# Optimization experiments

Hardware: AMD Instinct MI355X
Metric: run time of the kernel (lower is better)

Reference implementation:

```python
import jax, jax.numpy as jnp
import numpy as np

DIM = 256
NEG_SLOPE = 0.01  # torch F.leaky_relu default


def setup_inputs() -> dict:
    key = jax.random.key(0)
    ks = jax.random.split(key, 10)
    B, O, I, D = 16, 64, 512, DIM
    q = jax.random.normal(ks[0], (B, O, D), dtype=jnp.float32)
    k = jax.random.normal(ks[1], (B, I, D), dtype=jnp.float32)
    v = jax.random.normal(ks[2], (B, I, D), dtype=jnp.float32)
    mask = jax.random.randint(ks[3], (B, I), 0, 2).astype(bool)  # 1/True = pad
    s = 1.0 / np.sqrt(2 * D)
    # score MLP: Linear(2D -> D), tanh, Linear(D -> 1)
    W1 = jax.random.normal(ks[4], (D, 2 * D), dtype=jnp.float32) * s
    b1 = jnp.zeros((D,), dtype=jnp.float32)
    W2 = jax.random.normal(ks[5], (1, D), dtype=jnp.float32) * (1.0 / np.sqrt(D))
    b2 = jnp.zeros((1,), dtype=jnp.float32)
    # output projection fw: Linear(D -> D)
    Wf = jax.random.normal(ks[6], (D, D), dtype=jnp.float32) * (1.0 / np.sqrt(D))
    bf = jnp.zeros((D,), dtype=jnp.float32)
    return {"q": q, "k": k, "v": v, "mask": mask,
            "W1": W1, "b1": b1, "W2": W2, "b2": b2, "Wf": Wf, "bf": bf}


def reference(q, k, v, mask, W1, b1, W2, b2, Wf, bf):
    # Linear over concat([q, k]) decomposes exactly: W1 @ [q;k] = W1q@q + W1k@k
    D = q.shape[-1]
    W1q, W1k = W1[:, :D], W1[:, D:]
    qp = jnp.einsum('bod,hd->boh', q, W1q)          # (B, O, D)
    kp = jnp.einsum('bid,hd->bih', k, W1k)          # (B, I, D)
    h = jnp.tanh(qp[:, :, None, :] + kp[:, None, :, :] + b1)  # (B, O, I, D)
    score = jnp.einsum('boih,h->boi', h, W2[0]) + b2[0]       # (B, O, I)
    score = jnp.where(mask[:, None, :], -jnp.inf, score)
    attn = jax.nn.softmax(score, axis=-1)           # (B, O, I)
    out = jnp.einsum('boi,bid->bod', attn, v)       # (B, O, D)
    out = out @ Wf.T + bf                           # dropout in eval mode = identity
    out = jnp.where(out >= 0, out, NEG_SLOPE * out) # leaky_relu
    return out, attn
```

## Files before the change

### kernel.cpp

```cpp
#include <hip/hip_runtime.h>
#include <math.h>

#define DIM 256
#define BATCH 16
#define NO 64
#define NI 512
#define NEG_SLOPE 0.01f
#define CSCALE 2.885390081777927f
#define OT 2

__global__ __launch_bounds__(256, 4) void proj_kernel(
    const float* __restrict__ q, const float* __restrict__ k,
    const float* __restrict__ W1, const float* __restrict__ b1,
    const float* __restrict__ Wf,
    float* __restrict__ Eq, float* __restrict__ Ek4, float* __restrict__ WfT)
{
  __shared__ float smem[8704];

  const int t  = threadIdx.x;
  const int bx = blockIdx.x;

  if (bx >= 576) {
    const int tt = bx - 576;
    const int tr = tt >> 2, tc = tt & 3;
#pragma unroll
    for (int p = 0; p < 4; ++p) {
      int idx = p * 256 + t;
      int row = idx >> 4, j = idx & 15;
      float4 vv = *(const float4*)(Wf + (size_t)(tr * 64 + row) * 256 + tc * 64 + j * 4);
      *(float4*)&smem[row * 68 + j * 4] = vv;
    }
    __syncthreads();
#pragma unroll
    for (int p = 0; p < 4; ++p) {
      int idx = p * 256 + t;
      int row = idx >> 4, j = idx & 15;
      float4 ov;
      ov.x = smem[(j * 4 + 0) * 68 + row];
      ov.y = smem[(j * 4 + 1) * 68 + row];
      ov.z = smem[(j * 4 + 2) * 68 + row];
      ov.w = smem[(j * 4 + 3) * 68 + row];
      *(float4*)(WfT + (size_t)(tc * 64 + row) * 256 + tr * 64 + j * 4) = ov;
    }
    return;
  }

  float* At = smem;
  float* Wt = smem + 4352;

  const int tx = t & 15;
  const int ty = t >> 4;
  const int mt = bx >> 2;
  const int nt = bx & 3;
  const int r0 = mt * 64;
  const int h0 = nt * 64;
  const bool isq = (r0 < BATCH * NO);
  const float* src = isq ? (q + (size_t)r0 * DIM)
                         : (k + (size_t)(r0 - BATCH * NO) * DIM);
  const int coff = isq ? 0 : DIM;

  float acc[4][4] = {};

  for (int c0 = 0; c0 < DIM; c0 += 64) {
    __syncthreads();
#pragma unroll
    for (int p = 0; p < 4; ++p) {
      int idx = p * 256 + t;
      int row = idx >> 4, j = idx & 15;
      float4 av = *(const float4*)(src + (size_t)row * DIM + c0 + j * 4);
      At[(4 * j + 0) * 68 + row] = av.x;
      At[(4 * j + 1) * 68 + row] = av.y;
      At[(4 * j + 2) * 68 + row] = av.z;
      At[(4 * j + 3) * 68 + row] = av.w;
      float4 wv = *(const float4*)(W1 + (size_t)(h0 + row) * (2 * DIM) + coff + c0 + j * 4);
      Wt[(4 * j + 0) * 68 + row] = wv.x;
      Wt[(4 * j + 1) * 68 + row] = wv.y;
      Wt[(4 * j + 2) * 68 + row] = wv.z;
      Wt[(4 * j + 3) * 68 + row] = wv.w;
    }
    __syncthreads();
#pragma unroll
    for (int dk = 0; dk < 64; ++dk) {
      float4 a4 = *(const float4*)&At[dk * 68 + ty * 4];
      float4 w4 = *(const float4*)&Wt[dk * 68 + tx * 4];
      const float ar[4] = {a4.x, a4.y, a4.z, a4.w};
      const float wr[4] = {w4.x, w4.y, w4.z, w4.w};
#pragma unroll
      for (int rr = 0; rr < 4; ++rr)
#pragma unroll
        for (int cc = 0; cc < 4; ++cc)
          acc[rr][cc] = fmaf(ar[rr], wr[cc], acc[rr][cc]);
    }
  }

  if (isq) {
    float4 bv = *(const float4*)(b1 + h0 + tx * 4);
    const float br[4] = {bv.x, bv.y, bv.z, bv.w};
#pragma unroll
    for (int rr = 0; rr < 4; ++rr) {
      int r = r0 + ty * 4 + rr;
      float4 ov;
      ov.x = __builtin_amdgcn_exp2f((acc[rr][0] + br[0]) * CSCALE);
      ov.y = __builtin_amdgcn_exp2f((acc[rr][1] + br[1]) * CSCALE);
      ov.z = __builtin_amdgcn_exp2f((acc[rr][2] + br[2]) * CSCALE);
      ov.w = __builtin_amdgcn_exp2f((acc[rr][3] + br[3]) * CSCALE);
      *(float4*)(Eq + (size_t)r * DIM + h0 + tx * 4) = ov;
    }
  } else {
    int ig0 = r0 - BATCH * NO;
    int b   = ig0 >> 9;
    int i0  = (ig0 & 511) + ty * 4;
    int hq0 = (h0 >> 2) + tx;
#pragma unroll
    for (int rr = 0; rr < 4; ++rr) {
      float4 ov;
      ov.x = __builtin_amdgcn_exp2f(acc[rr][0] * CSCALE);
      ov.y = __builtin_amdgcn_exp2f(acc[rr][1] * CSCALE);
      ov.z = __builtin_amdgcn_exp2f(acc[rr][2] * CSCALE);
      ov.w = __builtin_amdgcn_exp2f(acc[rr][3] * CSCALE);
      *(float4*)(Ek4 + ((size_t)(b * 64 + hq0) * NI + i0 + rr) * 4) = ov;
    }
  }
}

__device__ __forceinline__ void f4arr(float4 v, float* a) {
  a[0] = v.x; a[1] = v.y; a[2] = v.z; a[3] = v.w;
}

__global__ __launch_bounds__(512, 4) void attn_kernel(
    const float* __restrict__ Eq, const float* __restrict__ Ek4,
    const float* __restrict__ v, const int* __restrict__ mask,
    const float* __restrict__ W2, const float* __restrict__ b2,
    const float* __restrict__ WfT, const float* __restrict__ bf,
    float* __restrict__ out, float* __restrict__ attn_out)
{
  __shared__ float sc[OT][NI];
  __shared__ float pvp[8][OT][DIM];
  __shared__ float o0[OT][DIM];
  __shared__ float red4[8][OT];
  __shared__ float redw[8];

  const int t    = threadIdx.x;
  const int lane = t & 63;
  const int wid  = t >> 6;

  const int blk  = blockIdx.x;
  const int tile = (blk & 7) * 64 + (blk >> 3);
  const int b    = tile >> 5;
  const int bo0  = b * 64 + (tile & 31) * OT;

  float partial = (t < DIM) ? W2[t] : 0.f;
#pragma unroll
  for (int off = 32; off >= 1; off >>= 1) partial += __shfl_xor(partial, off, 64);
  if (lane == 0) redw[wid] = partial;
  __syncthreads();
  float sumw2 = 0.f;
#pragma unroll
  for (int w = 0; w < 8; ++w) sumw2 += redw[w];
  const float base = sumw2 + b2[0];

  const int i = t;
  const float4* kb4 = (const float4*)Ek4 + (size_t)b * 64 * NI;
  const float* qrow0 = Eq + (size_t)(bo0 + 0) * DIM;
  const float* qrow1 = Eq + (size_t)(bo0 + 1) * DIM;

  float acc0 = 0.f, acc1 = 0.f;
#pragma unroll 8
  for (int hq = 0; hq < 64; ++hq) {
    float4 kq = kb4[(size_t)hq * NI + i];
    float wr[4], q0r[4], q1r[4], kv[4];
    f4arr(*(const float4*)(W2 + hq * 4), wr);
    f4arr(*(const float4*)(qrow0 + hq * 4), q0r);
    f4arr(*(const float4*)(qrow1 + hq * 4), q1r);
    f4arr(kq, kv);
#pragma unroll
    for (int pr = 0; pr < 2; ++pr) {
      const int ea = pr * 2, eb = pr * 2 + 1;
      float A0 = fmaf(q0r[ea], kv[ea], 1.f);
      float B0 = fmaf(q0r[eb], kv[eb], 1.f);
      float N0 = fmaf(wr[eb], A0, wr[ea] * B0);
      acc0 = fmaf(N0, __builtin_amdgcn_rcpf(A0 * B0), acc0);
      float A1 = fmaf(q1r[ea], kv[ea], 1.f);
      float B1 = fmaf(q1r[eb], kv[eb], 1.f);
      float N1 = fmaf(wr[eb], A1, wr[ea] * B1);
      acc1 = fmaf(N1, __builtin_amdgcn_rcpf(A1 * B1), acc1);
    }
  }

  const int mv = mask[(size_t)b * NI + i];
  float s0 = base - 2.f * acc0;
  float s1 = base - 2.f * acc1;
  if (mv) { s0 = -INFINITY; s1 = -INFINITY; }

  float p0 = __builtin_amdgcn_exp2f(s0 * 1.4426950408889634f);
  float p1 = __builtin_amdgcn_exp2f(s1 * 1.4426950408889634f);
  float ps0 = p0, ps1 = p1;
#pragma unroll
  for (int off = 32; off >= 1; off >>= 1) {
    ps0 += __shfl_xor(ps0, off, 64);
    ps1 += __shfl_xor(ps1, off, 64);
  }
  __syncthreads();
  if (lane == 0) { red4[wid][0] = ps0; red4[wid][1] = ps1; }
  __syncthreads();
  float ss0 = 0.f, ss1 = 0.f;
#pragma unroll
  for (int w = 0; w < 8; ++w) { ss0 += red4[w][0]; ss1 += red4[w][1]; }
  const float a0 = p0 * __builtin_amdgcn_rcpf(ss0);
  const float a1 = p1 * __builtin_amdgcn_rcpf(ss1);
  sc[0][i] = a0;
  sc[1][i] = a1;
  attn_out[(size_t)(bo0 + 0) * NI + i] = a0;
  attn_out[(size_t)(bo0 + 1) * NI + i] = a1;
  __syncthreads();

  {
    const int d4 = lane;
    float4 av0 = {0.f, 0.f, 0.f, 0.f};
    float4 av1 = {0.f, 0.f, 0.f, 0.f};
    const float4* vb4 = (const float4*)(v + (size_t)b * NI * DIM);
#pragma unroll 2
    for (int ib = wid * 64; ib < wid * 64 + 64; ib += 4) {
      float sa0[4], sa1[4];
      f4arr(*(const float4*)&sc[0][ib], sa0);
      f4arr(*(const float4*)&sc[1][ib], sa1);
#pragma unroll
      for (int j = 0; j < 4; ++j) {
        float4 vv = vb4[(size_t)(ib + j) * 64 + d4];
        av0.x = fmaf(sa0[j], vv.x, av0.x);
        av0.y = fmaf(sa0[j], vv.y, av0.y);
        av0.z = fmaf(sa0[j], vv.z, av0.z);
        av0.w = fmaf(sa0[j], vv.w, av0.w);
        av1.x = fmaf(sa1[j], vv.x, av1.x);
        av1.y = fmaf(sa1[j], vv.y, av1.y);
        av1.z = fmaf(sa1[j], vv.z, av1.z);
        av1.w = fmaf(sa1[j], vv.w, av1.w);
      }
    }
    *(float4*)&pvp[wid][0][d4 * 4] = av0;
    *(float4*)&pvp[wid][1][d4 * 4] = av1;
  }
  __syncthreads();
  {
    int oo = t >> 8, d = t & 255;
    float sacc = 0.f;
#pragma unroll
    for (int w = 0; w < 8; ++w) sacc += pvp[w][oo][d];
    o0[oo][d] = sacc;
  }
  __syncthreads();

  if (t < DIM) {
    const int d = t;
    float f0 = 0.f, f1 = 0.f;
#pragma unroll 8
    for (int e4 = 0; e4 < 64; ++e4) {
      float oa[4], ob[4];
      f4arr(*(const float4*)&o0[0][e4 * 4], oa);
      f4arr(*(const float4*)&o0[1][e4 * 4], ob);
#pragma unroll
      for (int c = 0; c < 4; ++c) {
        float wv = WfT[(size_t)(e4 * 4 + c) * DIM + d];
        f0 = fmaf(oa[c], wv, f0);
        f1 = fmaf(ob[c], wv, f1);
      }
    }
    float bfv = bf[d];
    f0 += bfv; f1 += bfv;
    f0 = (f0 >= 0.f) ? f0 : NEG_SLOPE * f0;
    f1 = (f1 >= 0.f) ? f1 : NEG_SLOPE * f1;
    out[(size_t)(bo0 + 0) * DIM + d] = f0;
    out[(size_t)(bo0 + 1) * DIM + d] = f1;
  }
}

extern "C" void kernel_launch(void* const* d_in, const int* in_sizes, int n_in,
                              void* d_out, int out_size, void* d_ws, size_t ws_size,
                              hipStream_t stream) {
  const float* q    = (const float*)d_in[0];
  const float* k    = (const float*)d_in[1];
  const float* v    = (const float*)d_in[2];
  const int*   mask = (const int*)d_in[3];
  const float* W1   = (const float*)d_in[4];
  const float* b1   = (const float*)d_in[5];
  const float* W2   = (const float*)d_in[6];
  const float* b2   = (const float*)d_in[7];
  const float* Wf   = (const float*)d_in[8];
  const float* bf   = (const float*)d_in[9];

  float* out      = (float*)d_out;
  float* attn_out = out + (size_t)BATCH * NO * DIM;

  float* Eq  = (float*)d_ws;
  float* Ek4 = Eq + (size_t)BATCH * NO * DIM;
  float* WfT = Ek4 + (size_t)BATCH * DIM * NI;

  proj_kernel<<<592, 256, 0, stream>>>(q, k, W1, b1, Wf, Eq, Ek4, WfT);
  attn_kernel<<<(BATCH * NO) / OT, 512, 0, stream>>>(Eq, Ek4, v, mask, W2, b2,
                                                     WfT, bf, out, attn_out);
}
```

Measured before the change: 142.4 us.

## Process four query rows per attention block with 1024 threads

Each attention block now handles four output rows instead of two, using 1024 threads split into two halves that each compute scores for two rows. The V-weighted sum and the output projection then reuse every V and WfT load across four rows, halving the global traffic for those operands. In exchange the grid shrinks to 256 blocks with one block per CU allowed, and the score phase still reads Ek4 separately in each half, so occupancy and latency hiding may drop.

After: 153.9 us. 8.1% more time.

```diff
diff --git a/kernel.cpp b/kernel.cpp
--- a/kernel.cpp
+++ b/kernel.cpp
@@ -7,7 +7,6 @@
 #define NI 512
 #define NEG_SLOPE 0.01f
 #define CSCALE 2.885390081777927f
-#define OT 2
 
 __global__ __launch_bounds__(256, 4) void proj_kernel(
     const float* __restrict__ q, const float* __restrict__ k,
@@ -127,27 +126,29 @@
   a[0] = v.x; a[1] = v.y; a[2] = v.z; a[3] = v.w;
 }
 
-__global__ __launch_bounds__(512, 4) void attn_kernel(
+__global__ __launch_bounds__(1024, 1) void attn_kernel(
     const float* __restrict__ Eq, const float* __restrict__ Ek4,
     const float* __restrict__ v, const int* __restrict__ mask,
     const float* __restrict__ W2, const float* __restrict__ b2,
     const float* __restrict__ WfT, const float* __restrict__ bf,
     float* __restrict__ out, float* __restrict__ attn_out)
 {
-  __shared__ float sc[OT][NI];
-  __shared__ float pvp[8][OT][DIM];
-  __shared__ float o0[OT][DIM];
-  __shared__ float red4[8][OT];
-  __shared__ float redw[8];
+  __shared__ float sc[4][NI];
+  __shared__ float pvp[16][4][DIM];
+  __shared__ float o0[4][DIM];
+  __shared__ float red4[16][2];
+  __shared__ float redw[16];
 
   const int t    = threadIdx.x;
   const int lane = t & 63;
   const int wid  = t >> 6;
+  const int half = t >> 9;
+  const int i    = t & 511;
 
   const int blk  = blockIdx.x;
-  const int tile = (blk & 7) * 64 + (blk >> 3);
-  const int b    = tile >> 5;
-  const int bo0  = b * 64 + (tile & 31) * OT;
+  const int tile = (blk & 7) * 32 + (blk >> 3);
+  const int b    = tile >> 4;
+  const int bo0  = b * 64 + (tile & 15) * 4;
 
   float partial = (t < DIM) ? W2[t] : 0.f;
 #pragma unroll
@@ -156,13 +157,12 @@
   __syncthreads();
   float sumw2 = 0.f;
 #pragma unroll
-  for (int w = 0; w < 8; ++w) sumw2 += redw[w];
+  for (int w = 0; w < 16; ++w) sumw2 += redw[w];
   const float base = sumw2 + b2[0];
 
-  const int i = t;
   const float4* kb4 = (const float4*)Ek4 + (size_t)b * 64 * NI;
-  const float* qrow0 = Eq + (size_t)(bo0 + 0) * DIM;
-  const float* qrow1 = Eq + (size_t)(bo0 + 1) * DIM;
+  const float* qrow0 = Eq + (size_t)(bo0 + half * 2 + 0) * DIM;
+  const float* qrow1 = Eq + (size_t)(bo0 + half * 2 + 1) * DIM;
 
   float acc0 = 0.f, acc1 = 0.f;
 #pragma unroll 8
@@ -205,72 +205,83 @@
   __syncthreads();
   float ss0 = 0.f, ss1 = 0.f;
 #pragma unroll
-  for (int w = 0; w < 8; ++w) { ss0 += red4[w][0]; ss1 += red4[w][1]; }
+  for (int w = 0; w < 8; ++w) {
+    ss0 += red4[half * 8 + w][0];
+    ss1 += red4[half * 8 + w][1];
+  }
   const float a0 = p0 * __builtin_amdgcn_rcpf(ss0);
   const float a1 = p1 * __builtin_amdgcn_rcpf(ss1);
-  sc[0][i] = a0;
-  sc[1][i] = a1;
-  attn_out[(size_t)(bo0 + 0) * NI + i] = a0;
-  attn_out[(size_t)(bo0 + 1) * NI + i] = a1;
+  sc[half * 2 + 0][i] = a0;
+  sc[half * 2 + 1][i] = a1;
+  attn_out[(size_t)(bo0 + half * 2 + 0) * NI + i] = a0;
+  attn_out[(size_t)(bo0 + half * 2 + 1) * NI + i] = a1;
   __syncthreads();
 
   {
     const int d4 = lane;
-    float4 av0 = {0.f, 0.f, 0.f, 0.f};
-    float4 av1 = {0.f, 0.f, 0.f, 0.f};
+    float4 av[4];
+#pragma unroll
+    for (int oo = 0; oo < 4; ++oo) av[oo] = make_float4(0.f, 0.f, 0.f, 0.f);
     const float4* vb4 = (const float4*)(v + (size_t)b * NI * DIM);
 #pragma unroll 2
-    for (int ib = wid * 64; ib < wid * 64 + 64; ib += 4) {
-      float sa0[4], sa1[4];
-      f4arr(*(const float4*)&sc[0][ib], sa0);
-      f4arr(*(const float4*)&sc[1][ib], sa1);
+    for (int ib = wid * 32; ib < wid * 32 + 32; ib += 4) {
+      float sa[4][4];
+#pragma unroll
+      for (int oo = 0; oo < 4; ++oo) f4arr(*(const float4*)&sc[oo][ib], sa[oo]);
 #pragma unroll
       for (int j = 0; j < 4; ++j) {
         float4 vv = vb4[(size_t)(ib + j) * 64 + d4];
-        av0.x = fmaf(sa0[j], vv.x, av0.x);
-        av0.y = fmaf(sa0[j], vv.y, av0.y);
-        av0.z = fmaf(sa0[j], vv.z, av0.z);
-        av0.w = fmaf(sa0[j], vv.w, av0.w);
-        av1.x = fmaf(sa1[j], vv.x, av1.x);
-        av1.y = fmaf(sa1[j], vv.y, av1.y);
-        av1.z = fmaf(sa1[j], vv.z, av1.z);
-        av1.w = fmaf(sa1[j], vv.w, av1.w);
+#pragma unroll
+        for (int oo = 0; oo < 4; ++oo) {
+          av[oo].x = fmaf(sa[oo][j], vv.x, av[oo].x);
+          av[oo].y = fmaf(sa[oo][j], vv.y, av[oo].y);
+          av[oo].z = fmaf(sa[oo][j], vv.z, av[oo].z);
+          av[oo].w = fmaf(sa[oo][j], vv.w, av[oo].w);
+        }
       }
     }
-    *(float4*)&pvp[wid][0][d4 * 4] = av0;
-    *(float4*)&pvp[wid][1][d4 * 4] = av1;
+#pragma unroll
+    for (int oo = 0; oo < 4; ++oo) *(float4*)&pvp[wid][oo][d4 * 4] = av[oo];
   }
   __syncthreads();
   {
-    int oo = t >> 8, d = t & 255;
+    const int oo = t >> 8, d = t & 255;
     float sacc = 0.f;
 #pragma unroll
-    for (int w = 0; w < 8; ++w) sacc += pvp[w][oo][d];
+    for (int w = 0; w < 16; ++w) sacc += pvp[w][oo][d];
     o0[oo][d] = sacc;
   }
   __syncthreads();
 
   if (t < DIM) {
     const int d = t;
-    float f0 = 0.f, f1 = 0.f;
+    float f0 = 0.f, f1 = 0.f, f2 = 0.f, f3 = 0.f;
 #pragma unroll 8
     for (int e4 = 0; e4 < 64; ++e4) {
-      float oa[4], ob[4];
+      float oa[4], ob[4], oc[4], od[4];
       f4arr(*(const float4*)&o0[0][e4 * 4], oa);
       f4arr(*(const float4*)&o0[1][e4 * 4], ob);
+      f4arr(*(const float4*)&o0[2][e4 * 4], oc);
+      f4arr(*(const float4*)&o0[3][e4 * 4], od);
 #pragma unroll
       for (int c = 0; c < 4; ++c) {
         float wv = WfT[(size_t)(e4 * 4 + c) * DIM + d];
         f0 = fmaf(oa[c], wv, f0);
         f1 = fmaf(ob[c], wv, f1);
+        f2 = fmaf(oc[c], wv, f2);
+        f3 = fmaf(od[c], wv, f3);
       }
     }
     float bfv = bf[d];
-    f0 += bfv; f1 += bfv;
+    f0 += bfv; f1 += bfv; f2 += bfv; f3 += bfv;
     f0 = (f0 >= 0.f) ? f0 : NEG_SLOPE * f0;
     f1 = (f1 >= 0.f) ? f1 : NEG_SLOPE * f1;
+    f2 = (f2 >= 0.f) ? f2 : NEG_SLOPE * f2;
+    f3 = (f3 >= 0.f) ? f3 : NEG_SLOPE * f3;
     out[(size_t)(bo0 + 0) * DIM + d] = f0;
     out[(size_t)(bo0 + 1) * DIM + d] = f1;
+    out[(size_t)(bo0 + 2) * DIM + d] = f2;
+    out[(size_t)(bo0 + 3) * DIM + d] = f3;
   }
 }
 
@@ -296,6 +307,6 @@
   float* WfT = Ek4 + (size_t)BATCH * DIM * NI;
 
   proj_kernel<<<592, 256, 0, stream>>>(q, k, W1, b1, Wf, Eq, Ek4, WfT);
-  attn_kernel<<<(BATCH * NO) / OT, 512, 0, stream>>>(Eq, Ek4, v, mask, W2, b2,
+  attn_kernel<<<(BATCH * NO) / 4, 1024, 0, stream>>>(Eq, Ek4, v, mask, W2, b2,
                                                      WfT, bf, out, attn_out);
 }
```

## Compact unmasked keys and skip score and PV work for padded positions

Applied to the files above, without the earlier changes.

Adds a mask-scan kernel that computes, per batch, a compacted list of unmasked key indices, each position's compacted slot, and the unmasked count. The projection kernel writes Ek only for unmasked keys into compacted slots. The attention kernel runs the tanh-score loop only for waves that hold compacted keys and sums PV only over unmasked rows through an index gather, then scatters attention weights back to original positions. This removes roughly half the score and PV work on random masks, at the cost of an extra launch and indirect loads of v.

Measured after the change: 138.0 us, median of 2. 1.03x faster.

```diff
diff --git a/kernel.cpp b/kernel.cpp
--- a/kernel.cpp
+++ b/kernel.cpp
@@ -9,10 +9,34 @@
 #define CSCALE 2.885390081777927f
 #define OT 2
 
+__global__ __launch_bounds__(512) void mask_scan_kernel(
+    const int* __restrict__ mask, int* __restrict__ idx,
+    int* __restrict__ posArr, int* __restrict__ cnt)
+{
+  __shared__ int wtot[8];
+  __shared__ int woff[8];
+  const int b = blockIdx.x, t = threadIdx.x;
+  const int lane = t & 63, wid = t >> 6;
+  const int unm = (mask[b * NI + t] == 0) ? 1 : 0;
+  unsigned long long bal = __ballot(unm);
+  int my  = __popcll(bal & ((1ull << lane) - 1ull));
+  if (lane == 0) wtot[wid] = __popcll(bal);
+  __syncthreads();
+  if (t == 0) {
+    int acc = 0;
+    for (int w = 0; w < 8; ++w) { woff[w] = acc; acc += wtot[w]; }
+    cnt[b] = acc;
+  }
+  __syncthreads();
+  int pos = woff[wid] + my;
+  if (unm) idx[b * NI + pos] = t;
+  posArr[b * NI + t] = unm ? pos : -1;
+}
+
 __global__ __launch_bounds__(256, 4) void proj_kernel(
     const float* __restrict__ q, const float* __restrict__ k,
     const float* __restrict__ W1, const float* __restrict__ b1,
-    const float* __restrict__ Wf,
+    const float* __restrict__ Wf, const int* __restrict__ posArr,
     float* __restrict__ Eq, float* __restrict__ Ek4, float* __restrict__ WfT)
 {
   __shared__ float smem[8704];
@@ -25,16 +49,16 @@
     const int tr = tt >> 2, tc = tt & 3;
 #pragma unroll
     for (int p = 0; p < 4; ++p) {
-      int idx = p * 256 + t;
-      int row = idx >> 4, j = idx & 15;
+      int idx2 = p * 256 + t;
+      int row = idx2 >> 4, j = idx2 & 15;
       float4 vv = *(const float4*)(Wf + (size_t)(tr * 64 + row) * 256 + tc * 64 + j * 4);
       *(float4*)&smem[row * 68 + j * 4] = vv;
     }
     __syncthreads();
 #pragma unroll
     for (int p = 0; p < 4; ++p) {
-      int idx = p * 256 + t;
-      int row = idx >> 4, j = idx & 15;
+      int idx2 = p * 256 + t;
+      int row = idx2 >> 4, j = idx2 & 15;
       float4 ov;
       ov.x = smem[(j * 4 + 0) * 68 + row];
       ov.y = smem[(j * 4 + 1) * 68 + row];
@@ -65,8 +89,8 @@
     __syncthreads();
 #pragma unroll
     for (int p = 0; p < 4; ++p) {
-      int idx = p * 256 + t;
-      int row = idx >> 4, j = idx & 15;
+      int idx2 = p * 256 + t;
+      int row = idx2 >> 4, j = idx2 & 15;
       float4 av = *(const float4*)(src + (size_t)row * DIM + c0 + j * 4);
       At[(4 * j + 0) * 68 + row] = av.x;
       At[(4 * j + 1) * 68 + row] = av.y;
@@ -113,12 +137,15 @@
     int hq0 = (h0 >> 2) + tx;
 #pragma unroll
     for (int rr = 0; rr < 4; ++rr) {
-      float4 ov;
-      ov.x = __builtin_amdgcn_exp2f(acc[rr][0] * CSCALE);
-      ov.y = __builtin_amdgcn_exp2f(acc[rr][1] * CSCALE);
-      ov.z = __builtin_amdgcn_exp2f(acc[rr][2] * CSCALE);
-      ov.w = __builtin_amdgcn_exp2f(acc[rr][3] * CSCALE);
-      *(float4*)(Ek4 + ((size_t)(b * 64 + hq0) * NI + i0 + rr) * 4) = ov;
+      int pos = posArr[b * NI + i0 + rr];
+      if (pos >= 0) {
+        float4 ov;
+        ov.x = __builtin_amdgcn_exp2f(acc[rr][0] * CSCALE);
+        ov.y = __builtin_amdgcn_exp2f(acc[rr][1] * CSCALE);
+        ov.z = __builtin_amdgcn_exp2f(acc[rr][2] * CSCALE);
+        ov.w = __builtin_amdgcn_exp2f(acc[rr][3] * CSCALE);
+        *(float4*)(Ek4 + ((size_t)(b * 64 + hq0) * NI + pos) * 4) = ov;
+      }
     }
   }
 }
@@ -129,12 +156,14 @@
 
 __global__ __launch_bounds__(512, 4) void attn_kernel(
     const float* __restrict__ Eq, const float* __restrict__ Ek4,
-    const float* __restrict__ v, const int* __restrict__ mask,
+    const float* __restrict__ v, const int* __restrict__ idx,
+    const int* __restrict__ posArr, const int* __restrict__ cnt,
     const float* __restrict__ W2, const float* __restrict__ b2,
     const float* __restrict__ WfT, const float* __restrict__ bf,
     float* __restrict__ out, float* __restrict__ attn_out)
 {
   __shared__ float sc[OT][NI];
+  __shared__ int   idxs[NI];
   __shared__ float pvp[8][OT][DIM];
   __shared__ float o0[OT][DIM];
   __shared__ float red4[8][OT];
@@ -149,6 +178,10 @@
   const int b    = tile >> 5;
   const int bo0  = b * 64 + (tile & 31) * OT;
 
+  const int cntb = cnt[b];
+  idxs[t] = idx[b * NI + t];
+  const int myPos = posArr[b * NI + t];
+
   float partial = (t < DIM) ? W2[t] : 0.f;
 #pragma unroll
   for (int off = 32; off >= 1; off >>= 1) partial += __shfl_xor(partial, off, 64);
@@ -159,38 +192,40 @@
   for (int w = 0; w < 8; ++w) sumw2 += redw[w];
   const float base = sumw2 + b2[0];
 
-  const int i = t;
+  const int j = t;
+  const bool active = (j < cntb);
+  const int jc = active ? j : (cntb > 0 ? cntb - 1 : 0);
   const float4* kb4 = (const float4*)Ek4 + (size_t)b * 64 * NI;
   const float* qrow0 = Eq + (size_t)(bo0 + 0) * DIM;
   const float* qrow1 = Eq + (size_t)(bo0 + 1) * DIM;
 
   float acc0 = 0.f, acc1 = 0.f;
+  if (wid * 64 < cntb) {
 #pragma unroll 8
-  for (int hq = 0; hq < 64; ++hq) {
-    float4 kq = kb4[(size_t)hq * NI + i];
-    float wr[4], q0r[4], q1r[4], kv[4];
-    f4arr(*(const float4*)(W2 + hq * 4), wr);
-    f4arr(*(const float4*)(qrow0 + hq * 4), q0r);
-    f4arr(*(const float4*)(qrow1 + hq * 4), q1r);
-    f4arr(kq, kv);
-#pragma unroll
-    for (int pr = 0; pr < 2; ++pr) {
-      const int ea = pr * 2, eb = pr * 2 + 1;
-      float A0 = fmaf(q0r[ea], kv[ea], 1.f);
-      float B0 = fmaf(q0r[eb], kv[eb], 1.f);
-      float N0 = fmaf(wr[eb], A0, wr[ea] * B0);
-      acc0 = fmaf(N0, __builtin_amdgcn_rcpf(A0 * B0), acc0);
-      float A1 = fmaf(q1r[ea], kv[ea], 1.f);
-      float B1 = fmaf(q1r[eb], kv[eb], 1.f);
-      float N1 = fmaf(wr[eb], A1, wr[ea] * B1);
-      acc1 = fmaf(N1, __builtin_amdgcn_rcpf(A1 * B1), acc1);
-    }
-  }
-
-  const int mv = mask[(size_t)b * NI + i];
-  float s0 = base - 2.f * acc0;
-  float s1 = base - 2.f * acc1;
-  if (mv) { s0 = -INFINITY; s1 = -INFINITY; }
+    for (int hq = 0; hq < 64; ++hq) {
+      float4 kq = kb4[(size_t)hq * NI + jc];
+      float wr[4], q0r[4], q1r[4], kv[4];
+      f4arr(*(const float4*)(W2 + hq * 4), wr);
+      f4arr(*(const float4*)(qrow0 + hq * 4), q0r);
+      f4arr(*(const float4*)(qrow1 + hq * 4), q1r);
+      f4arr(kq, kv);
+#pragma unroll
+      for (int pr = 0; pr < 2; ++pr) {
+        const int ea = pr * 2, eb = pr * 2 + 1;
+        float A0 = fmaf(q0r[ea], kv[ea], 1.f);
+        float B0 = fmaf(q0r[eb], kv[eb], 1.f);
+        float N0 = fmaf(wr[eb], A0, wr[ea] * B0);
+        acc0 = fmaf(N0, __builtin_amdgcn_rcpf(A0 * B0), acc0);
+        float A1 = fmaf(q1r[ea], kv[ea], 1.f);
+        float B1 = fmaf(q1r[eb], kv[eb], 1.f);
+        float N1 = fmaf(wr[eb], A1, wr[ea] * B1);
+        acc1 = fmaf(N1, __builtin_amdgcn_rcpf(A1 * B1), acc1);
+      }
+    }
+  }
+
+  float s0 = active ? (base - 2.f * acc0) : -INFINITY;
+  float s1 = active ? (base - 2.f * acc1) : -INFINITY;
 
   float p0 = __builtin_amdgcn_exp2f(s0 * 1.4426950408889634f);
   float p1 = __builtin_amdgcn_exp2f(s1 * 1.4426950408889634f);
@@ -208,34 +243,36 @@
   for (int w = 0; w < 8; ++w) { ss0 += red4[w][0]; ss1 += red4[w][1]; }
   const float a0 = p0 * __builtin_amdgcn_rcpf(ss0);
   const float a1 = p1 * __builtin_amdgcn_rcpf(ss1);
-  sc[0][i] = a0;
-  sc[1][i] = a1;
-  attn_out[(size_t)(bo0 + 0) * NI + i] = a0;
-  attn_out[(size_t)(bo0 + 1) * NI + i] = a1;
-  __syncthreads();
+  sc[0][j] = a0;
+  sc[1][j] = a1;
+  __syncthreads();
+
+  {
+    float w0 = (myPos >= 0) ? sc[0][myPos] : 0.f;
+    float w1 = (myPos >= 0) ? sc[1][myPos] : 0.f;
+    attn_out[(size_t)(bo0 + 0) * NI + t] = w0;
+    attn_out[(size_t)(bo0 + 1) * NI + t] = w1;
+  }
 
   {
     const int d4 = lane;
     float4 av0 = {0.f, 0.f, 0.f, 0.f};
     float4 av1 = {0.f, 0.f, 0.f, 0.f};
     const float4* vb4 = (const float4*)(v + (size_t)b * NI * DIM);
-#pragma unroll 2
-    for (int ib = wid * 64; ib < wid * 64 + 64; ib += 4) {
-      float sa0[4], sa1[4];
-      f4arr(*(const float4*)&sc[0][ib], sa0);
-      f4arr(*(const float4*)&sc[1][ib], sa1);
-#pragma unroll
-      for (int j = 0; j < 4; ++j) {
-        float4 vv = vb4[(size_t)(ib + j) * 64 + d4];
-        av0.x = fmaf(sa0[j], vv.x, av0.x);
-        av0.y = fmaf(sa0[j], vv.y, av0.y);
-        av0.z = fmaf(sa0[j], vv.z, av0.z);
-        av0.w = fmaf(sa0[j], vv.w, av0.w);
-        av1.x = fmaf(sa1[j], vv.x, av1.x);
-        av1.y = fmaf(sa1[j], vv.y, av1.y);
-        av1.z = fmaf(sa1[j], vv.z, av1.z);
-        av1.w = fmaf(sa1[j], vv.w, av1.w);
-      }
+    const int jend = min(wid * 64 + 64, cntb);
+#pragma unroll 4
+    for (int jb = wid * 64; jb < jend; ++jb) {
+      int row = idxs[jb];
+      float sa0 = sc[0][jb], sa1 = sc[1][jb];
+      float4 vv = vb4[(size_t)row * 64 + d4];
+      av0.x = fmaf(sa0, vv.x, av0.x);
+      av0.y = fmaf(sa0, vv.y, av0.y);
+      av0.z = fmaf(sa0, vv.z, av0.z);
+      av0.w = fmaf(sa0, vv.w, av0.w);
+      av1.x = fmaf(sa1, vv.x, av1.x);
+      av1.y = fmaf(sa1, vv.y, av1.y);
+      av1.z = fmaf(sa1, vv.z, av1.z);
+      av1.w = fmaf(sa1, vv.w, av1.w);
     }
     *(float4*)&pvp[wid][0][d4 * 4] = av0;
     *(float4*)&pvp[wid][1][d4 * 4] = av1;
@@ -291,11 +328,15 @@
   float* out      = (float*)d_out;
   float* attn_out = out + (size_t)BATCH * NO * DIM;
 
-  float* Eq  = (float*)d_ws;
-  float* Ek4 = Eq + (size_t)BATCH * NO * DIM;
-  float* WfT = Ek4 + (size_t)BATCH * DIM * NI;
-
-  proj_kernel<<<592, 256, 0, stream>>>(q, k, W1, b1, Wf, Eq, Ek4, WfT);
-  attn_kernel<<<(BATCH * NO) / OT, 512, 0, stream>>>(Eq, Ek4, v, mask, W2, b2,
-                                                     WfT, bf, out, attn_out);
-}
+  float* Eq   = (float*)d_ws;
+  float* Ek4  = Eq + (size_t)BATCH * NO * DIM;
+  float* WfT  = Ek4 + (size_t)BATCH * DIM * NI;
+  int*   idx  = (int*)(WfT + (size_t)DIM * DIM);
+  int*   pos  = idx + BATCH * NI;
+  int*   cnt  = pos + BATCH * NI;
+
+  mask_scan_kernel<<<BATCH, 512, 0, stream>>>(mask, idx, pos, cnt);
+  proj_kernel<<<592, 256, 0, stream>>>(q, k, W1, b1, Wf, pos, Eq, Ek4, WfT);
+  attn_kernel<<<(BATCH * NO) / OT, 512, 0, stream>>>(Eq, Ek4, v, idx, pos, cnt,
+                                                     W2, b2, WfT, bf, out, attn_out);
+}
```
